# Kernel tuning notes

Measured on AMD Instinct MI355X. Metric: run time of the kernel, lower is better.

The kernel has to match this reference:

```python
import jax, jax.numpy as jnp
import numpy as np
from jax import lax

D = 1024  # inputSize == hidden size
B = 128   # batch
T = 256   # step


def setup_inputs() -> dict:
    key = jax.random.key(0)
    ks = jax.random.split(key, 9)
    s = 1.0 / np.sqrt(D)  # torch LSTMCell/Linear default init scale
    return {
        "inp": jax.random.normal(ks[0], (B, T, D), dtype=jnp.float32),
        "h0": jnp.zeros((B, D), dtype=jnp.float32),
        "c0": jnp.zeros((B, D), dtype=jnp.float32),
        "W_ih": jax.random.uniform(ks[1], (4 * D, D), jnp.float32, -s, s),
        "W_hh": jax.random.uniform(ks[2], (4 * D, D), jnp.float32, -s, s),
        "b_ih": jax.random.uniform(ks[3], (4 * D,), jnp.float32, -s, s),
        "b_hh": jax.random.uniform(ks[4], (4 * D,), jnp.float32, -s, s),
        "fc_w": jax.random.uniform(ks[5], (1, D), jnp.float32, -s, s),
        "fc_b": jax.random.uniform(ks[6], (1,), jnp.float32, -s, s),
        "step": T,
    }


def reference(inp, h0, c0, W_ih, W_hh, b_ih, b_hh, fc_w, fc_b, step):
    # The original's double python loop just transposes [B, T, D] -> [T, B, D].
    xs = jnp.swapaxes(inp, 0, 1)  # [T, B, D]

    def cell(carry, x):
        h, c = carry
        # torch.nn.LSTMCell gate order: i, f, g, o
        gates = x @ W_ih.T + b_ih + h @ W_hh.T + b_hh  # [B, 4D]
        i, f, g, o = jnp.split(gates, 4, axis=-1)
        i = jax.nn.sigmoid(i)
        f = jax.nn.sigmoid(f)
        g = jnp.tanh(g)
        o = jax.nn.sigmoid(o)
        c2 = f * c + i * g
        h2 = o * jnp.tanh(c2)
        return (h2, c2), None

    (hx, cx), _ = lax.scan(cell, (h0, c0), xs)
    yhat = jax.nn.sigmoid(hx @ fc_w.T + fc_b)  # [B, 1]
    return (yhat, hx, cx)
```

## Files before the change

kernel.cpp:

```cpp
#include <hip/hip_runtime.h>
#include <hip/hip_cooperative_groups.h>

namespace cg = cooperative_groups;

#define Dd 1024
#define Bb 128
#define Tt 256
#define NWG 256
#define NTHR 256

typedef short bf16x8 __attribute__((ext_vector_type(8)));
typedef float f32x4 __attribute__((ext_vector_type(4)));
typedef unsigned int u32x4 __attribute__((ext_vector_type(4)));
typedef unsigned long long u64;

static __device__ __forceinline__ unsigned short f2bf(float x) {
  unsigned int u = __float_as_uint(x);
  u += 0x7fffu + ((u >> 16) & 1u);
  return (unsigned short)(u >> 16);
}
static __device__ __forceinline__ unsigned int pk2(float a, float b) {
  return (unsigned int)f2bf(a) | ((unsigned int)f2bf(b) << 16);
}
static __device__ __forceinline__ bf16x8 as_bf(uint4 u) {
  union { uint4 u; bf16x8 v; } x; x.u = u; return x.v;
}
static __device__ __forceinline__ f32x4 mfma_(bf16x8 a, bf16x8 b, f32x4 c) {
  return __builtin_amdgcn_mfma_f32_16x16x32_bf16(a, b, c, 0, 0, 0);
}
static __device__ __forceinline__ float sigm(float x) { return 1.f / (1.f + __expf(-x)); }
static __device__ __forceinline__ float tanh_s(float x) { return 1.f - 2.f / (__expf(2.f * x) + 1.f); }
static __device__ __forceinline__ u64 aload(const u64* p) {
  return __hip_atomic_load(p, __ATOMIC_RELAXED, __HIP_MEMORY_SCOPE_AGENT);
}

template<int RING>
__global__ void __launch_bounds__(NTHR, 1) lstm_kernel(
    const float* __restrict__ inp, const float* __restrict__ h0,
    const float* __restrict__ c0, const float* __restrict__ W_ih,
    const float* __restrict__ W_hh, const float* __restrict__ b_ih,
    const float* __restrict__ b_hh, const float* __restrict__ fc_w,
    const float* __restrict__ fc_b, float* __restrict__ out,
    int* __restrict__ flags, unsigned short* __restrict__ hbuf,
    unsigned short* __restrict__ xbf, int use_xbf)
{
  extern __shared__ uint4 ldsW[];
  __shared__ float red[4];
  __shared__ int sent;

  const int tid = threadIdx.x;
  const int wg  = blockIdx.x;
  const int gid = wg * NTHR + tid;
  cg::grid_group grid = cg::this_grid();

  const int gs = wg >> 1;
  const int bh = wg & 1;

  if (tid < 4)
    __hip_atomic_store(&flags[bh * 512 + gs * 4 + tid], 0,
                       __ATOMIC_RELAXED, __HIP_MEMORY_SCOPE_AGENT);
  if (tid == 0) sent = -1;

  if (use_xbf) {
    for (int i = gid; i < Tt * Bb * (Dd / 8); i += NWG * NTHR) {
      int d8 = i & 127, b = (i >> 7) & 127, t = i >> 14;
      const float* s = inp + ((size_t)b * Tt + t) * Dd + d8 * 8;
      uint4 p;
      p.x = pk2(s[0], s[1]); p.y = pk2(s[2], s[3]);
      p.z = pk2(s[4], s[5]); p.w = pk2(s[6], s[7]);
      *(uint4*)(xbf + (size_t)i * 8) = p;
    }
  }
  uint4* hb4w = (uint4*)hbuf;
  for (int i = gid; i < 128 * 128; i += NWG * NTHR) {
    int row = i & 127, gsl = i >> 7;
    const float* s = h0 + (size_t)row * Dd + gsl * 8;
    uint4 p;
    p.x = pk2(s[0], s[1]); p.y = pk2(s[2], s[3]);
    p.z = pk2(s[4], s[5]); p.w = pk2(s[6], s[7]);
    hb4w[gsl * 128 + row] = p;
  }

  for (int i = tid; i < 8192; i += NTHR) {
    int l2 = i & 63, mmct = (i >> 6) & 3, kc = i >> 8;
    int cc = l2 & 15, ct = mmct & 1;
    int row = (((ct << 1) | (cc >> 3)) << 10) | (gs << 3) | (cc & 7);
    int k = kc * 32 + ((l2 >> 4) << 3);
    const float* s = ((mmct & 2) ? W_hh : W_ih) + (size_t)row * Dd + k;
    uint4 p;
    p.x = pk2(s[0], s[1]); p.y = pk2(s[2], s[3]);
    p.z = pk2(s[4], s[5]); p.w = pk2(s[6], s[7]);
    ldsW[i] = p;
  }

  const int w = tid >> 6, l = tid & 63;
  const int c = l & 15;
  const int rowbase = bh * 64 + w * 16;
  const int arow = rowbase + c;
  const int koff8 = l >> 4;
  const int r0 = ((c >> 3) << 10) | (gs << 3) | (c & 7);
  const int r1 = ((2 + (c >> 3)) << 10) | (gs << 3) | (c & 7);
  const float bias0 = b_ih[r0] + b_hh[r0];
  const float bias1 = b_ih[r1] + b_hh[r1];
  const int dim = (gs << 3) | (c & 7);
  const int crow = rowbase + (koff8 << 2);
  float creg[4];
  #pragma unroll
  for (int j = 0; j < 4; ++j) creg[j] = c0[(size_t)(crow + j) * Dd + dim];

  float* out_y = out;
  float* out_h = out + Bb;
  float* out_c = out + Bb + (size_t)Bb * Dd;

  int* myflag = &flags[bh * 512 + gs * 4 + w];
  const u64* fq = (const u64*)(flags + bh * 512);
  const int shbase = ((l & 15) >> 2) * 16;

  grid.sync();

  f32x4 pa0, pa1, pb0, pb1;

  {
    pa0 = f32x4{bias0, bias0, bias0, bias0};
    pa1 = f32x4{bias1, bias1, bias1, bias1};
    pb0 = f32x4{0.f, 0.f, 0.f, 0.f};
    pb1 = f32x4{0.f, 0.f, 0.f, 0.f};
    if (use_xbf) {
      const uint4* xA = (const uint4*)(xbf + ((size_t)0 * Bb + arow) * Dd + koff8 * 8);
      #pragma unroll
      for (int kc = 0; kc < 32; kc += 2) {
        uint4 ax0 = xA[kc * 4];
        uint4 ax1 = xA[(kc + 1) * 4];
        const int lb0 = kc * 256 + l, lb1 = (kc + 1) * 256 + l;
        pa0 = mfma_(as_bf(ax0), as_bf(ldsW[lb0]),      pa0);
        pa1 = mfma_(as_bf(ax0), as_bf(ldsW[lb0 + 64]), pa1);
        pb0 = mfma_(as_bf(ax1), as_bf(ldsW[lb1]),      pb0);
        pb1 = mfma_(as_bf(ax1), as_bf(ldsW[lb1 + 64]), pb1);
      }
    } else {
      const float* xF = inp + ((size_t)arow * Tt + 0) * Dd + koff8 * 8;
      #pragma unroll 4
      for (int kc = 0; kc < 32; ++kc) {
        const float* xs = xF + kc * 32;
        uint4 axu;
        axu.x = pk2(xs[0], xs[1]); axu.y = pk2(xs[2], xs[3]);
        axu.z = pk2(xs[4], xs[5]); axu.w = pk2(xs[6], xs[7]);
        const int lb = kc * 256 + l;
        pa0 = mfma_(as_bf(axu), as_bf(ldsW[lb]),      pa0);
        pa1 = mfma_(as_bf(axu), as_bf(ldsW[lb + 64]), pa1);
      }
    }
  }

  for (int t = 0; t < Tt; ++t) {
    const int rslot = RING ? t : (t & 1);
    const int wslot = RING ? (t + 1) : ((t + 1) & 1);

    if (w == 0) {
      int ok;
      do {
        u64 a = aload(&fq[l]);
        u64 b = aload(&fq[l + 64]);
        u64 c2 = aload(&fq[l + 128]);
        u64 d2 = aload(&fq[l + 192]);
        ok = ((int)a >= t) && ((int)(a >> 32) >= t) &&
             ((int)b >= t) && ((int)(b >> 32) >= t) &&
             ((int)c2 >= t) && ((int)(c2 >> 32) >= t) &&
             ((int)d2 >= t) && ((int)(d2 >> 32) >= t);
      } while (!__all(ok));
      __hip_atomic_store(&sent, t, __ATOMIC_RELEASE, __HIP_MEMORY_SCOPE_WORKGROUP);
    } else {
      while (__hip_atomic_load(&sent, __ATOMIC_ACQUIRE, __HIP_MEMORY_SCOPE_WORKGROUP) < t) {}
    }
    asm volatile("" ::: "memory");

    if constexpr (RING) {
      const uint4* hA4 = (const uint4*)(hbuf + (size_t)rslot * 131072);
      uint4 hc[8], hn[8];
      #pragma unroll
      for (int i = 0; i < 8; ++i) hc[i] = hA4[(i * 4 + koff8) * 128 + arow];
      #pragma unroll
      for (int oct = 0; oct < 4; ++oct) {
        if (oct < 3) {
          #pragma unroll
          for (int i = 0; i < 8; ++i)
            hn[i] = hA4[(((oct + 1) * 8 + i) * 4 + koff8) * 128 + arow];
        }
        #pragma unroll
        for (int i = 0; i < 8; i += 2) {
          const int kc = oct * 8 + i;
          const int lb0 = kc * 256 + l, lb1 = (kc + 1) * 256 + l;
          pa0 = mfma_(as_bf(hc[i]),     as_bf(ldsW[lb0 + 128]), pa0);
          pa1 = mfma_(as_bf(hc[i]),     as_bf(ldsW[lb0 + 192]), pa1);
          pb0 = mfma_(as_bf(hc[i + 1]), as_bf(ldsW[lb1 + 128]), pb0);
          pb1 = mfma_(as_bf(hc[i + 1]), as_bf(ldsW[lb1 + 192]), pb1);
        }
        if (oct < 3) {
          #pragma unroll
          for (int i = 0; i < 8; ++i) hc[i] = hn[i];
        }
      }
    } else {
      const u64* hA = (const u64*)hbuf + (size_t)rslot * 32768;
      #pragma unroll
      for (int kc = 0; kc < 32; kc += 2) {
        const int hi0 = (kc * 4 + koff8) * 256 + arow * 2;
        const int hi1 = ((kc + 1) * 4 + koff8) * 256 + arow * 2;
        union { u64 q[2]; uint4 p4; } h0u, h1u;
        h0u.q[0] = aload(&hA[hi0]); h0u.q[1] = aload(&hA[hi0 + 1]);
        h1u.q[0] = aload(&hA[hi1]); h1u.q[1] = aload(&hA[hi1 + 1]);
        const int lb0 = kc * 256 + l, lb1 = (kc + 1) * 256 + l;
        pa0 = mfma_(as_bf(h0u.p4), as_bf(ldsW[lb0 + 128]), pa0);
        pa1 = mfma_(as_bf(h0u.p4), as_bf(ldsW[lb0 + 192]), pa1);
        pb0 = mfma_(as_bf(h1u.p4), as_bf(ldsW[lb1 + 128]), pb0);
        pb1 = mfma_(as_bf(h1u.p4), as_bf(ldsW[lb1 + 192]), pb1);
      }
    }
    f32x4 acc0 = pa0 + pb0;
    f32x4 acc1 = pa1 + pb1;

    float fo0[4], fo1[4];
    #pragma unroll
    for (int j = 0; j < 4; ++j) {
      fo0[j] = __shfl_xor(acc0[j], 8);
      fo1[j] = __shfl_xor(acc1[j], 8);
    }
    unsigned int bfu0 = 0, bfu1 = 0, bfu2 = 0, bfu3 = 0;
    if (c < 8) {
      float hnv[4];
      #pragma unroll
      for (int j = 0; j < 4; ++j) {
        float iv = sigm(acc0[j]);
        float fv = sigm(fo0[j]);
        float gv = tanh_s(acc1[j]);
        float ov = sigm(fo1[j]);
        float cn = fv * creg[j] + iv * gv;
        float hn2 = ov * tanh_s(cn);
        creg[j] = cn;
        hnv[j] = hn2;
        if (t == Tt - 1) {
          size_t off = (size_t)(crow + j) * Dd + dim;
          __hip_atomic_store(&out_h[off], hn2, __ATOMIC_RELAXED, __HIP_MEMORY_SCOPE_AGENT);
          __hip_atomic_store(&out_c[off], cn, __ATOMIC_RELAXED, __HIP_MEMORY_SCOPE_AGENT);
        }
      }
      bfu0 = f2bf(hnv[0]); bfu1 = f2bf(hnv[1]);
      bfu2 = f2bf(hnv[2]); bfu3 = f2bf(hnv[3]);
    }

    unsigned int w0 = 0, w1 = 0, w2 = 0, w3 = 0;
    #pragma unroll
    for (int j = 0; j < 4; ++j) {
      unsigned int src = (j == 0) ? bfu0 : (j == 1) ? bfu1 : (j == 2) ? bfu2 : bfu3;
      unsigned int lo0 = __shfl((int)src, shbase + 0);
      unsigned int hi0g = __shfl((int)src, shbase + 1);
      unsigned int lo1 = __shfl((int)src, shbase + 2);
      unsigned int hi1g = __shfl((int)src, shbase + 3);
      unsigned int lo2 = __shfl((int)src, shbase + 4);
      unsigned int hi2g = __shfl((int)src, shbase + 5);
      unsigned int lo3 = __shfl((int)src, shbase + 6);
      unsigned int hi3g = __shfl((int)src, shbase + 7);
      bool mine = ((l & 3) == j);
      if (mine) {
        w0 = lo0 | (hi0g << 16);
        w1 = lo1 | (hi1g << 16);
        w2 = lo2 | (hi2g << 16);
        w3 = lo3 | (hi3g << 16);
      }
    }
    if (l < 16) {
      u32x4 val = {w0, w1, w2, w3};
      unsigned short* hw = hbuf + (size_t)wslot * 131072
                           + (size_t)gs * 1024 + (size_t)(rowbase + l) * 8;
      asm volatile("global_store_dwordx4 %0, %1, off sc0 sc1"
                   :: "v"(hw), "v"(val) : "memory");
    }

    pa0 = f32x4{bias0, bias0, bias0, bias0};
    pa1 = f32x4{bias1, bias1, bias1, bias1};
    pb0 = f32x4{0.f, 0.f, 0.f, 0.f};
    pb1 = f32x4{0.f, 0.f, 0.f, 0.f};
    if (t < Tt - 1) {
      if (use_xbf) {
        const uint4* xA = (const uint4*)(xbf + ((size_t)(t + 1) * Bb + arow) * Dd + koff8 * 8);
        #pragma unroll
        for (int kc = 0; kc < 32; kc += 2) {
          uint4 ax0 = xA[kc * 4];
          uint4 ax1 = xA[(kc + 1) * 4];
          const int lb0 = kc * 256 + l, lb1 = (kc + 1) * 256 + l;
          pa0 = mfma_(as_bf(ax0), as_bf(ldsW[lb0]),      pa0);
          pa1 = mfma_(as_bf(ax0), as_bf(ldsW[lb0 + 64]), pa1);
          pb0 = mfma_(as_bf(ax1), as_bf(ldsW[lb1]),      pb0);
          pb1 = mfma_(as_bf(ax1), as_bf(ldsW[lb1 + 64]), pb1);
        }
      } else {
        const float* xF = inp + ((size_t)arow * Tt + (t + 1)) * Dd + koff8 * 8;
        #pragma unroll 4
        for (int kc = 0; kc < 32; ++kc) {
          const float* xs = xF + kc * 32;
          uint4 axu;
          axu.x = pk2(xs[0], xs[1]); axu.y = pk2(xs[2], xs[3]);
          axu.z = pk2(xs[4], xs[5]); axu.w = pk2(xs[6], xs[7]);
          const int lb = kc * 256 + l;
          pa0 = mfma_(as_bf(axu), as_bf(ldsW[lb]),      pa0);
          pa1 = mfma_(as_bf(axu), as_bf(ldsW[lb + 64]), pa1);
        }
      }
    }

    asm volatile("s_waitcnt vmcnt(0)" ::: "memory");
    if (l == 0)
      __hip_atomic_store(myflag, t + 1, __ATOMIC_RELAXED, __HIP_MEMORY_SCOPE_AGENT);
  }

  if (wg < Bb) {
    {
      const u64* fa = (const u64*)flags;
      int ok;
      do {
        ok = 1;
        #pragma unroll
        for (int r = 0; r < 8; ++r) {
          u64 v = aload(&fa[l + r * 64]);
          ok &= ((int)v >= Tt) && ((int)(v >> 32) >= Tt);
        }
      } while (!__all(ok));
    }
    const u64* hr = (const u64*)(out_h + (size_t)wg * Dd);
    float s = 0.f;
    for (int k = tid; k < Dd / 2; k += NTHR) {
      u64 v = aload(&hr[k]);
      union { u64 u; float f[2]; } q; q.u = v;
      s += q.f[0] * fc_w[2 * k] + q.f[1] * fc_w[2 * k + 1];
    }
    #pragma unroll
    for (int off = 32; off > 0; off >>= 1) s += __shfl_down(s, off);
    if (l == 0) red[w] = s;
    __syncthreads();
    if (tid == 0) {
      float tot = red[0] + red[1] + red[2] + red[3] + fc_b[0];
      out_y[wg] = sigm(tot);
    }
  }
}

extern "C" void kernel_launch(void* const* d_in, const int* in_sizes, int n_in,
                              void* d_out, int out_size, void* d_ws, size_t ws_size,
                              hipStream_t stream) {
  (void)in_sizes; (void)n_in; (void)out_size;
  const float* inp  = (const float*)d_in[0];
  const float* h0   = (const float*)d_in[1];
  const float* c0   = (const float*)d_in[2];
  const float* W_ih = (const float*)d_in[3];
  const float* W_hh = (const float*)d_in[4];
  const float* b_ih = (const float*)d_in[5];
  const float* b_hh = (const float*)d_in[6];
  const float* fc_w = (const float*)d_in[7];
  const float* fc_b = (const float*)d_in[8];
  float* out = (float*)d_out;

  const size_t fbytes = 16384;
  const size_t slot   = (size_t)Bb * Dd * 2;
  const size_t ring1  = (size_t)(Tt + 1) * slot;
  const size_t ring0  = 2 * slot;
  const size_t xbytes = (size_t)Tt * Bb * Dd * 2;

  int ring, use_xbf;
  size_t rbytes;
  if (ws_size >= fbytes + ring1 + xbytes)      { ring = 1; use_xbf = 1; rbytes = ring1; }
  else if (ws_size >= fbytes + ring1)          { ring = 1; use_xbf = 0; rbytes = ring1; }
  else if (ws_size >= fbytes + ring0 + xbytes) { ring = 0; use_xbf = 1; rbytes = ring0; }
  else                                         { ring = 0; use_xbf = 0; rbytes = ring0; }

  int* flags = (int*)d_ws;
  unsigned short* hbuf = (unsigned short*)((char*)d_ws + fbytes);
  unsigned short* xbf  = (unsigned short*)((char*)d_ws + fbytes + rbytes);

  void* kfn = ring ? (void*)lstm_kernel<1> : (void*)lstm_kernel<0>;
  (void)hipFuncSetAttribute((const void*)kfn,
                            hipFuncAttributeMaxDynamicSharedMemorySize, 131072);

  void* kargs[] = {(void*)&inp, (void*)&h0, (void*)&c0, (void*)&W_ih, (void*)&W_hh,
                   (void*)&b_ih, (void*)&b_hh, (void*)&fc_w, (void*)&fc_b,
                   (void*)&out, (void*)&flags, (void*)&hbuf, (void*)&xbf, (void*)&use_xbf};
  (void)hipLaunchCooperativeKernel(kfn, dim3(NWG), dim3(NTHR),
                                   kargs, 131072u, stream);
}
```

Measured before the change: 2.914 ms.

## Merge batch halves into one 512-thread workgroup per gate slice

Switches from 256 workgroups of 256 threads, where each pair split the batch in half, to 128 workgroups of 512 threads, where each covers the full batch for its gate slice. This halves the number of flags each step barrier polls and shares the LDS weight tile across all 128 batch rows, which should lower global sync cost per timestep. It also drops the register-prefetched double-buffered h loads in favour of simple per-iteration loads. In exchange only 128 CUs are used, so per-CU MFMA and LDS work doubles, and h load latency may be less hidden.

```diff
diff --git a/kernel.cpp b/kernel.cpp
--- a/kernel.cpp
+++ b/kernel.cpp
@@ -6,8 +6,8 @@
 #define Dd 1024
 #define Bb 128
 #define Tt 256
-#define NWG 256
-#define NTHR 256
+#define NWG 128
+#define NTHR 512
 
 typedef short bf16x8 __attribute__((ext_vector_type(8)));
 typedef float f32x4 __attribute__((ext_vector_type(4)));
@@ -45,7 +45,7 @@
     unsigned short* __restrict__ xbf, int use_xbf)
 {
   extern __shared__ uint4 ldsW[];
-  __shared__ float red[4];
+  __shared__ float red[8];
   __shared__ int sent;
 
   const int tid = threadIdx.x;
@@ -53,11 +53,10 @@
   const int gid = wg * NTHR + tid;
   cg::grid_group grid = cg::this_grid();
 
-  const int gs = wg >> 1;
-  const int bh = wg & 1;
-
-  if (tid < 4)
-    __hip_atomic_store(&flags[bh * 512 + gs * 4 + tid], 0,
+  const int gs = wg;
+
+  if (tid < 8)
+    __hip_atomic_store(&flags[gs * 8 + tid], 0,
                        __ATOMIC_RELAXED, __HIP_MEMORY_SCOPE_AGENT);
   if (tid == 0) sent = -1;
 
@@ -95,7 +94,7 @@
 
   const int w = tid >> 6, l = tid & 63;
   const int c = l & 15;
-  const int rowbase = bh * 64 + w * 16;
+  const int rowbase = w * 16;
   const int arow = rowbase + c;
   const int koff8 = l >> 4;
   const int r0 = ((c >> 3) << 10) | (gs << 3) | (c & 7);
@@ -112,8 +111,8 @@
   float* out_h = out + Bb;
   float* out_c = out + Bb + (size_t)Bb * Dd;
 
-  int* myflag = &flags[bh * 512 + gs * 4 + w];
-  const u64* fq = (const u64*)(flags + bh * 512);
+  int* myflag = &flags[gs * 8 + w];
+  const u64* fq = (const u64*)flags;
   const int shbase = ((l & 15) >> 2) * 16;
 
   grid.sync();
@@ -161,12 +160,8 @@
       do {
         u64 a = aload(&fq[l]);
         u64 b = aload(&fq[l + 64]);
-        u64 c2 = aload(&fq[l + 128]);
-        u64 d2 = aload(&fq[l + 192]);
         ok = ((int)a >= t) && ((int)(a >> 32) >= t) &&
-             ((int)b >= t) && ((int)(b >> 32) >= t) &&
-             ((int)c2 >= t) && ((int)(c2 >> 32) >= t) &&
-             ((int)d2 >= t) && ((int)(d2 >> 32) >= t);
+             ((int)b >= t) && ((int)(b >> 32) >= t);
       } while (!__all(ok));
       __hip_atomic_store(&sent, t, __ATOMIC_RELEASE, __HIP_MEMORY_SCOPE_WORKGROUP);
     } else {
@@ -176,29 +171,15 @@
 
     if constexpr (RING) {
       const uint4* hA4 = (const uint4*)(hbuf + (size_t)rslot * 131072);
-      uint4 hc[8], hn[8];
-      #pragma unroll
-      for (int i = 0; i < 8; ++i) hc[i] = hA4[(i * 4 + koff8) * 128 + arow];
-      #pragma unroll
-      for (int oct = 0; oct < 4; ++oct) {
-        if (oct < 3) {
-          #pragma unroll
-          for (int i = 0; i < 8; ++i)
-            hn[i] = hA4[(((oct + 1) * 8 + i) * 4 + koff8) * 128 + arow];
-        }
-        #pragma unroll
-        for (int i = 0; i < 8; i += 2) {
-          const int kc = oct * 8 + i;
-          const int lb0 = kc * 256 + l, lb1 = (kc + 1) * 256 + l;
-          pa0 = mfma_(as_bf(hc[i]),     as_bf(ldsW[lb0 + 128]), pa0);
-          pa1 = mfma_(as_bf(hc[i]),     as_bf(ldsW[lb0 + 192]), pa1);
-          pb0 = mfma_(as_bf(hc[i + 1]), as_bf(ldsW[lb1 + 128]), pb0);
-          pb1 = mfma_(as_bf(hc[i + 1]), as_bf(ldsW[lb1 + 192]), pb1);
-        }
-        if (oct < 3) {
-          #pragma unroll
-          for (int i = 0; i < 8; ++i) hc[i] = hn[i];
-        }
+      #pragma unroll
+      for (int kc = 0; kc < 32; kc += 2) {
+        uint4 h0u = hA4[(kc * 4 + koff8) * 128 + arow];
+        uint4 h1u = hA4[((kc + 1) * 4 + koff8) * 128 + arow];
+        const int lb0 = kc * 256 + l, lb1 = (kc + 1) * 256 + l;
+        pa0 = mfma_(as_bf(h0u), as_bf(ldsW[lb0 + 128]), pa0);
+        pa1 = mfma_(as_bf(h0u), as_bf(ldsW[lb0 + 192]), pa1);
+        pb0 = mfma_(as_bf(h1u), as_bf(ldsW[lb1 + 128]), pb0);
+        pb1 = mfma_(as_bf(h1u), as_bf(ldsW[lb1 + 192]), pb1);
       }
     } else {
       const u64* hA = (const u64*)hbuf + (size_t)rslot * 32768;
@@ -313,17 +294,14 @@
       __hip_atomic_store(myflag, t + 1, __ATOMIC_RELAXED, __HIP_MEMORY_SCOPE_AGENT);
   }
 
-  if (wg < Bb) {
+  {
     {
-      const u64* fa = (const u64*)flags;
       int ok;
       do {
-        ok = 1;
-        #pragma unroll
-        for (int r = 0; r < 8; ++r) {
-          u64 v = aload(&fa[l + r * 64]);
-          ok &= ((int)v >= Tt) && ((int)(v >> 32) >= Tt);
-        }
+        u64 a = aload(&fq[l]);
+        u64 b = aload(&fq[l + 64]);
+        ok = ((int)a >= Tt) && ((int)(a >> 32) >= Tt) &&
+             ((int)b >= Tt) && ((int)(b >> 32) >= Tt);
       } while (!__all(ok));
     }
     const u64* hr = (const u64*)(out_h + (size_t)wg * Dd);
@@ -338,7 +316,9 @@
     if (l == 0) red[w] = s;
     __syncthreads();
     if (tid == 0) {
-      float tot = red[0] + red[1] + red[2] + red[3] + fc_b[0];
+      float tot = fc_b[0];
+      #pragma unroll
+      for (int i = 0; i < 8; ++i) tot += red[i];
       out_y[wg] = sigm(tot);
     }
   }
```

Result: slower. 4.622 ms (+58.6%).

## Precompute input projection in separate kernel, leaving only recurrent GEMM in scan

Applied to the files above, without the earlier changes.

Splits the monolithic LSTM kernel into three launches: a fp32-to-bf16 conversion of the input, a kernel that computes x@W_ih^T + biases for all timesteps into a bf16 gate buffer, and a cooperative scan kernel that only does h@W_hh^T per step and adds the precomputed gates. This takes the input-projection GEMM off the sequential critical path and halves the LDS weight footprint in the scan. The cost is extra global traffic for a large gate buffer, added launches, and an extra bf16 rounding of the input gates. It only runs when the workspace is large enough, otherwise it falls back to the old kernel. The ring path in the fallback also loses its hand-written h prefetch.

```diff
diff --git a/kernel.cpp b/kernel.cpp
--- a/kernel.cpp
+++ b/kernel.cpp
@@ -22,6 +22,9 @@
 static __device__ __forceinline__ unsigned int pk2(float a, float b) {
   return (unsigned int)f2bf(a) | ((unsigned int)f2bf(b) << 16);
 }
+static __device__ __forceinline__ float bf2f(unsigned int ubits) {
+  return __uint_as_float(ubits << 16);
+}
 static __device__ __forceinline__ bf16x8 as_bf(uint4 u) {
   union { uint4 u; bf16x8 v; } x; x.u = u; return x.v;
 }
@@ -34,8 +37,294 @@
   return __hip_atomic_load(p, __ATOMIC_RELAXED, __HIP_MEMORY_SCOPE_AGENT);
 }
 
+__global__ void xcvt_kernel(const float* __restrict__ inp,
+                            unsigned short* __restrict__ xbf)
+{
+  for (int i = blockIdx.x * 256 + threadIdx.x; i < Tt * Bb * (Dd / 8);
+       i += gridDim.x * 256) {
+    int d8 = i & 127, b = (i >> 7) & 127, t = i >> 14;
+    const float* s = inp + ((size_t)b * Tt + t) * Dd + d8 * 8;
+    uint4 p;
+    p.x = pk2(s[0], s[1]); p.y = pk2(s[2], s[3]);
+    p.z = pk2(s[4], s[5]); p.w = pk2(s[6], s[7]);
+    *(uint4*)(xbf + (size_t)i * 8) = p;
+  }
+}
+
+__global__ void __launch_bounds__(256, 1) xg_kernel(
+    const unsigned short* __restrict__ xbf, const float* __restrict__ W_ih,
+    const float* __restrict__ b_ih, const float* __restrict__ b_hh,
+    unsigned short* __restrict__ xg)
+{
+  extern __shared__ uint4 ldsW[];
+  const int tid = threadIdx.x;
+  const int wg  = blockIdx.x;
+  const int gs = wg >> 1;
+  const int bh = wg & 1;
+
+  for (int i = tid; i < 4096; i += 256) {
+    int l2 = i & 63, ct = (i >> 6) & 1, kc = i >> 7;
+    int cc = l2 & 15;
+    int row = (((ct << 1) | (cc >> 3)) << 10) | (gs << 3) | (cc & 7);
+    int k = kc * 32 + ((l2 >> 4) << 3);
+    const float* s = W_ih + (size_t)row * Dd + k;
+    uint4 p;
+    p.x = pk2(s[0], s[1]); p.y = pk2(s[2], s[3]);
+    p.z = pk2(s[4], s[5]); p.w = pk2(s[6], s[7]);
+    ldsW[i] = p;
+  }
+  __syncthreads();
+
+  const int w = tid >> 6, l = tid & 63;
+  const int c = l & 15;
+  const int rowbase = bh * 64 + w * 16;
+  const int arow = rowbase + c;
+  const int koff8 = l >> 4;
+  const int r0 = ((c >> 3) << 10) | (gs << 3) | (c & 7);
+  const int r1 = ((2 + (c >> 3)) << 10) | (gs << 3) | (c & 7);
+  const float bias0 = b_ih[r0] + b_hh[r0];
+  const float bias1 = b_ih[r1] + b_hh[r1];
+  const int crow = rowbase + (koff8 << 2);
+
+  for (int t = 0; t < Tt; ++t) {
+    f32x4 a0 = {bias0, bias0, bias0, bias0};
+    f32x4 a1 = {bias1, bias1, bias1, bias1};
+    f32x4 e0 = {0.f, 0.f, 0.f, 0.f};
+    f32x4 e1 = {0.f, 0.f, 0.f, 0.f};
+    const uint4* xA = (const uint4*)(xbf + ((size_t)t * Bb + arow) * Dd + koff8 * 8);
+    #pragma unroll
+    for (int kc = 0; kc < 32; kc += 2) {
+      uint4 ax0 = xA[kc * 4];
+      uint4 ax1 = xA[(kc + 1) * 4];
+      const int lb0 = kc * 128 + l, lb1 = (kc + 1) * 128 + l;
+      a0 = mfma_(as_bf(ax0), as_bf(ldsW[lb0]),      a0);
+      a1 = mfma_(as_bf(ax0), as_bf(ldsW[lb0 + 64]), a1);
+      e0 = mfma_(as_bf(ax1), as_bf(ldsW[lb1]),      e0);
+      e1 = mfma_(as_bf(ax1), as_bf(ldsW[lb1 + 64]), e1);
+    }
+    f32x4 s0 = a0 + e0;
+    f32x4 s1 = a1 + e1;
+    u64 q0 = (u64)pk2(s0[0], s0[1]) | ((u64)pk2(s0[2], s0[3]) << 32);
+    u64 q1 = (u64)pk2(s1[0], s1[1]) | ((u64)pk2(s1[2], s1[3]) << 32);
+    *(u64*)(xg + (size_t)t * 524288 + (size_t)r0 * 128 + crow) = q0;
+    *(u64*)(xg + (size_t)t * 524288 + (size_t)r1 * 128 + crow) = q1;
+  }
+}
+
+__global__ void __launch_bounds__(256, 1) lstm_scan_kernel(
+    const float* __restrict__ h0, const float* __restrict__ c0,
+    const float* __restrict__ W_hh, const float* __restrict__ fc_w,
+    const float* __restrict__ fc_b, float* __restrict__ out,
+    int* __restrict__ flags, unsigned short* __restrict__ hbuf,
+    const unsigned short* __restrict__ xg)
+{
+  extern __shared__ uint4 ldsW[];
+  __shared__ float red[4];
+  __shared__ int sent;
+
+  const int tid = threadIdx.x;
+  const int wg  = blockIdx.x;
+  const int gid = wg * 256 + tid;
+  cg::grid_group grid = cg::this_grid();
+
+  const int gs = wg >> 1;
+  const int bh = wg & 1;
+
+  if (tid < 4)
+    __hip_atomic_store(&flags[bh * 512 + gs * 4 + tid], 0,
+                       __ATOMIC_RELAXED, __HIP_MEMORY_SCOPE_AGENT);
+  if (tid == 0) sent = -1;
+
+  uint4* hb4w = (uint4*)hbuf;
+  for (int i = gid; i < 128 * 128; i += NWG * 256) {
+    int row = i & 127, gsl = i >> 7;
+    const float* s = h0 + (size_t)row * Dd + gsl * 8;
+    uint4 p;
+    p.x = pk2(s[0], s[1]); p.y = pk2(s[2], s[3]);
+    p.z = pk2(s[4], s[5]); p.w = pk2(s[6], s[7]);
+    hb4w[gsl * 128 + row] = p;
+  }
+
+  for (int i = tid; i < 4096; i += 256) {
+    int l2 = i & 63, ct = (i >> 6) & 1, kc = i >> 7;
+    int cc = l2 & 15;
+    int row = (((ct << 1) | (cc >> 3)) << 10) | (gs << 3) | (cc & 7);
+    int k = kc * 32 + ((l2 >> 4) << 3);
+    const float* s = W_hh + (size_t)row * Dd + k;
+    uint4 p;
+    p.x = pk2(s[0], s[1]); p.y = pk2(s[2], s[3]);
+    p.z = pk2(s[4], s[5]); p.w = pk2(s[6], s[7]);
+    ldsW[i] = p;
+  }
+
+  const int w = tid >> 6, l = tid & 63;
+  const int c = l & 15;
+  const int rowbase = bh * 64 + w * 16;
+  const int arow = rowbase + c;
+  const int koff8 = l >> 4;
+  const int r0 = ((c >> 3) << 10) | (gs << 3) | (c & 7);
+  const int r1 = ((2 + (c >> 3)) << 10) | (gs << 3) | (c & 7);
+  const int dim = (gs << 3) | (c & 7);
+  const int crow = rowbase + (koff8 << 2);
+  float creg[4];
+  #pragma unroll
+  for (int j = 0; j < 4; ++j) creg[j] = c0[(size_t)(crow + j) * Dd + dim];
+
+  float* out_y = out;
+  float* out_h = out + Bb;
+  float* out_c = out + Bb + (size_t)Bb * Dd;
+
+  int* myflag = &flags[bh * 512 + gs * 4 + w];
+  const u64* fq = (const u64*)(flags + bh * 512);
+  const int shbase = ((l & 15) >> 2) * 16;
+
+  grid.sync();
+
+  u64 xq0 = *(const u64*)(xg + (size_t)r0 * 128 + crow);
+  u64 xq1 = *(const u64*)(xg + (size_t)r1 * 128 + crow);
+
+  for (int t = 0; t < Tt; ++t) {
+    if (w == 0) {
+      int ok;
+      do {
+        u64 a = aload(&fq[l]);
+        u64 b = aload(&fq[l + 64]);
+        u64 c2 = aload(&fq[l + 128]);
+        u64 d2 = aload(&fq[l + 192]);
+        ok = ((int)a >= t) && ((int)(a >> 32) >= t) &&
+             ((int)b >= t) && ((int)(b >> 32) >= t) &&
+             ((int)c2 >= t) && ((int)(c2 >> 32) >= t) &&
+             ((int)d2 >= t) && ((int)(d2 >> 32) >= t);
+      } while (!__all(ok));
+      __hip_atomic_store(&sent, t, __ATOMIC_RELEASE, __HIP_MEMORY_SCOPE_WORKGROUP);
+    } else {
+      while (__hip_atomic_load(&sent, __ATOMIC_ACQUIRE, __HIP_MEMORY_SCOPE_WORKGROUP) < t) {}
+    }
+    asm volatile("" ::: "memory");
+
+    f32x4 pa0 = {0.f, 0.f, 0.f, 0.f};
+    f32x4 pa1 = {0.f, 0.f, 0.f, 0.f};
+    f32x4 pb0 = {0.f, 0.f, 0.f, 0.f};
+    f32x4 pb1 = {0.f, 0.f, 0.f, 0.f};
+    {
+      const uint4* hA4 = (const uint4*)(hbuf + (size_t)t * 131072);
+      #pragma unroll
+      for (int kc = 0; kc < 32; kc += 2) {
+        uint4 h0u = hA4[(kc * 4 + koff8) * 128 + arow];
+        uint4 h1u = hA4[((kc + 1) * 4 + koff8) * 128 + arow];
+        const int lb0 = kc * 128 + l, lb1 = (kc + 1) * 128 + l;
+        pa0 = mfma_(as_bf(h0u), as_bf(ldsW[lb0]),      pa0);
+        pa1 = mfma_(as_bf(h0u), as_bf(ldsW[lb0 + 64]), pa1);
+        pb0 = mfma_(as_bf(h1u), as_bf(ldsW[lb1]),      pb0);
+        pb1 = mfma_(as_bf(h1u), as_bf(ldsW[lb1 + 64]), pb1);
+      }
+    }
+    f32x4 acc0 = pa0 + pb0;
+    f32x4 acc1 = pa1 + pb1;
+    #pragma unroll
+    for (int j = 0; j < 4; ++j) {
+      acc0[j] += bf2f((unsigned int)(xq0 >> (16 * j)) & 0xffffu);
+      acc1[j] += bf2f((unsigned int)(xq1 >> (16 * j)) & 0xffffu);
+    }
+
+    float fo0[4], fo1[4];
+    #pragma unroll
+    for (int j = 0; j < 4; ++j) {
+      fo0[j] = __shfl_xor(acc0[j], 8);
+      fo1[j] = __shfl_xor(acc1[j], 8);
+    }
+    unsigned int bfu0 = 0, bfu1 = 0, bfu2 = 0, bfu3 = 0;
+    if (c < 8) {
+      float hnv[4];
+      #pragma unroll
+      for (int j = 0; j < 4; ++j) {
+        float iv = sigm(acc0[j]);
+        float fv = sigm(fo0[j]);
+        float gv = tanh_s(acc1[j]);
+        float ov = sigm(fo1[j]);
+        float cn = fv * creg[j] + iv * gv;
+        float hn2 = ov * tanh_s(cn);
+        creg[j] = cn;
+        hnv[j] = hn2;
+        if (t == Tt - 1) {
+          size_t off = (size_t)(crow + j) * Dd + dim;
+          __hip_atomic_store(&out_h[off], hn2, __ATOMIC_RELAXED, __HIP_MEMORY_SCOPE_AGENT);
+          __hip_atomic_store(&out_c[off], cn, __ATOMIC_RELAXED, __HIP_MEMORY_SCOPE_AGENT);
+        }
+      }
+      bfu0 = f2bf(hnv[0]); bfu1 = f2bf(hnv[1]);
+      bfu2 = f2bf(hnv[2]); bfu3 = f2bf(hnv[3]);
+    }
+
+    unsigned int w0 = 0, w1 = 0, w2 = 0, w3 = 0;
+    #pragma unroll
+    for (int j = 0; j < 4; ++j) {
+      unsigned int src = (j == 0) ? bfu0 : (j == 1) ? bfu1 : (j == 2) ? bfu2 : bfu3;
+      unsigned int lo0 = __shfl((int)src, shbase + 0);
+      unsigned int hi0g = __shfl((int)src, shbase + 1);
+      unsigned int lo1 = __shfl((int)src, shbase + 2);
+      unsigned int hi1g = __shfl((int)src, shbase + 3);
+      unsigned int lo2 = __shfl((int)src, shbase + 4);
+      unsigned int hi2g = __shfl((int)src, shbase + 5);
+      unsigned int lo3 = __shfl((int)src, shbase + 6);
+      unsigned int hi3g = __shfl((int)src, shbase + 7);
+      bool mine = ((l & 3) == j);
+      if (mine) {
+        w0 = lo0 | (hi0g << 16);
+        w1 = lo1 | (hi1g << 16);
+        w2 = lo2 | (hi2g << 16);
+        w3 = lo3 | (hi3g << 16);
+      }
+    }
+    if (l < 16) {
+      u32x4 val = {w0, w1, w2, w3};
+      unsigned short* hw = hbuf + (size_t)(t + 1) * 131072
+                           + (size_t)gs * 1024 + (size_t)(rowbase + l) * 8;
+      asm volatile("global_store_dwordx4 %0, %1, off sc0 sc1"
+                   :: "v"(hw), "v"(val) : "memory");
+    }
+    if (t + 1 < Tt) {
+      xq0 = *(const u64*)(xg + (size_t)(t + 1) * 524288 + (size_t)r0 * 128 + crow);
+      xq1 = *(const u64*)(xg + (size_t)(t + 1) * 524288 + (size_t)r1 * 128 + crow);
+    }
+    asm volatile("s_waitcnt vmcnt(0)" ::: "memory");
+    if (l == 0)
+      __hip_atomic_store(myflag, t + 1, __ATOMIC_RELAXED, __HIP_MEMORY_SCOPE_AGENT);
+  }
+
+  if (wg < Bb) {
+    {
+      const u64* fa = (const u64*)flags;
+      int ok;
+      do {
+        ok = 1;
+        #pragma unroll
+        for (int r = 0; r < 8; ++r) {
+          u64 v = aload(&fa[l + r * 64]);
+          ok &= ((int)v >= Tt) && ((int)(v >> 32) >= Tt);
+        }
+      } while (!__all(ok));
+    }
+    const u64* hr = (const u64*)(out_h + (size_t)wg * Dd);
+    float s = 0.f;
+    for (int k = tid; k < Dd / 2; k += 256) {
+      u64 v = aload(&hr[k]);
+      union { u64 u; float f[2]; } q; q.u = v;
+      s += q.f[0] * fc_w[2 * k] + q.f[1] * fc_w[2 * k + 1];
+    }
+    #pragma unroll
+    for (int off = 32; off > 0; off >>= 1) s += __shfl_down(s, off);
+    if (l == 0) red[w] = s;
+    __syncthreads();
+    if (tid == 0) {
+      float tot = red[0] + red[1] + red[2] + red[3] + fc_b[0];
+      out_y[wg] = sigm(tot);
+    }
+  }
+}
+
 template<int RING>
-__global__ void __launch_bounds__(NTHR, 1) lstm_kernel(
+__global__ void __launch_bounds__(NTHR, 1) lstm_kernel_mono(
     const float* __restrict__ inp, const float* __restrict__ h0,
     const float* __restrict__ c0, const float* __restrict__ W_ih,
     const float* __restrict__ W_hh, const float* __restrict__ b_ih,
@@ -80,7 +369,6 @@
     p.z = pk2(s[4], s[5]); p.w = pk2(s[6], s[7]);
     hb4w[gsl * 128 + row] = p;
   }
-
   for (int i = tid; i < 8192; i += NTHR) {
     int l2 = i & 63, mmct = (i >> 6) & 3, kc = i >> 8;
     int cc = l2 & 15, ct = mmct & 1;
@@ -119,7 +407,6 @@
   grid.sync();
 
   f32x4 pa0, pa1, pb0, pb1;
-
   {
     pa0 = f32x4{bias0, bias0, bias0, bias0};
     pa1 = f32x4{bias1, bias1, bias1, bias1};
@@ -176,29 +463,15 @@
 
     if constexpr (RING) {
       const uint4* hA4 = (const uint4*)(hbuf + (size_t)rslot * 131072);
-      uint4 hc[8], hn[8];
       #pragma unroll
-      for (int i = 0; i < 8; ++i) hc[i] = hA4[(i * 4 + koff8) * 128 + arow];
-      #pragma unroll
-      for (int oct = 0; oct < 4; ++oct) {
-        if (oct < 3) {
-          #pragma unroll
-          for (int i = 0; i < 8; ++i)
-            hn[i] = hA4[(((oct + 1) * 8 + i) * 4 + koff8) * 128 + arow];
-        }
-        #pragma unroll
-        for (int i = 0; i < 8; i += 2) {
-          const int kc = oct * 8 + i;
-          const int lb0 = kc * 256 + l, lb1 = (kc + 1) * 256 + l;
-          pa0 = mfma_(as_bf(hc[i]),     as_bf(ldsW[lb0 + 128]), pa0);
-          pa1 = mfma_(as_bf(hc[i]),     as_bf(ldsW[lb0 + 192]), pa1);
-          pb0 = mfma_(as_bf(hc[i + 1]), as_bf(ldsW[lb1 + 128]), pb0);
-          pb1 = mfma_(as_bf(hc[i + 1]), as_bf(ldsW[lb1 + 192]), pb1);
-        }
-        if (oct < 3) {
-          #pragma unroll
-          for (int i = 0; i < 8; ++i) hc[i] = hn[i];
-        }
+      for (int kc = 0; kc < 32; kc += 2) {
+        uint4 h0u = hA4[(kc * 4 + koff8) * 128 + arow];
+        uint4 h1u = hA4[((kc + 1) * 4 + koff8) * 128 + arow];
+        const int lb0 = kc * 256 + l, lb1 = (kc + 1) * 256 + l;
+        pa0 = mfma_(as_bf(h0u), as_bf(ldsW[lb0 + 128]), pa0);
+        pa1 = mfma_(as_bf(h0u), as_bf(ldsW[lb0 + 192]), pa1);
+        pb0 = mfma_(as_bf(h1u), as_bf(ldsW[lb1 + 128]), pb0);
+        pb1 = mfma_(as_bf(h1u), as_bf(ldsW[lb1 + 192]), pb1);
       }
     } else {
       const u64* hA = (const u64*)hbuf + (size_t)rslot * 32768;
@@ -359,11 +632,37 @@
   const float* fc_b = (const float*)d_in[8];
   float* out = (float*)d_out;
 
-  const size_t fbytes = 16384;
-  const size_t slot   = (size_t)Bb * Dd * 2;
-  const size_t ring1  = (size_t)(Tt + 1) * slot;
-  const size_t ring0  = 2 * slot;
-  const size_t xbytes = (size_t)Tt * Bb * Dd * 2;
+  const size_t fbytes  = 16384;
+  const size_t slot    = (size_t)Bb * Dd * 2;
+  const size_t ring1   = (size_t)(Tt + 1) * slot;
+  const size_t ring0   = 2 * slot;
+  const size_t xbytes  = (size_t)Tt * Bb * Dd * 2;
+  const size_t xgbytes = (size_t)Tt * 4096 * Bb * 2;
+
+  int* flags = (int*)d_ws;
+  unsigned short* hbuf = (unsigned short*)((char*)d_ws + fbytes);
+
+  if (ws_size >= fbytes + ring1 + xgbytes + xbytes) {
+    unsigned short* xg  = (unsigned short*)((char*)d_ws + fbytes + ring1);
+    unsigned short* xbf = (unsigned short*)((char*)d_ws + fbytes + ring1 + xgbytes);
+
+    hipLaunchKernelGGL(xcvt_kernel, dim3(2048), dim3(256), 0, stream, inp, xbf);
+
+    (void)hipFuncSetAttribute((const void*)xg_kernel,
+                              hipFuncAttributeMaxDynamicSharedMemorySize, 65536);
+    hipLaunchKernelGGL(xg_kernel, dim3(256), dim3(256), 65536, stream,
+                       xbf, W_ih, b_ih, b_hh, xg);
+
+    (void)hipFuncSetAttribute((const void*)lstm_scan_kernel,
+                              hipFuncAttributeMaxDynamicSharedMemorySize, 65536);
+    const unsigned short* xg_c = xg;
+    void* kargs[] = {(void*)&h0, (void*)&c0, (void*)&W_hh, (void*)&fc_w,
+                     (void*)&fc_b, (void*)&out, (void*)&flags, (void*)&hbuf,
+                     (void*)&xg_c};
+    (void)hipLaunchCooperativeKernel((void*)lstm_scan_kernel, dim3(NWG), dim3(NTHR),
+                                     kargs, 65536u, stream);
+    return;
+  }
 
   int ring, use_xbf;
   size_t rbytes;
@@ -372,11 +671,9 @@
   else if (ws_size >= fbytes + ring0 + xbytes) { ring = 0; use_xbf = 1; rbytes = ring0; }
   else                                         { ring = 0; use_xbf = 0; rbytes = ring0; }
 
-  int* flags = (int*)d_ws;
-  unsigned short* hbuf = (unsigned short*)((char*)d_ws + fbytes);
-  unsigned short* xbf  = (unsigned short*)((char*)d_ws + fbytes + rbytes);
-
-  void* kfn = ring ? (void*)lstm_kernel<1> : (void*)lstm_kernel<0>;
+  unsigned short* xbf = (unsigned short*)((char*)d_ws + fbytes + rbytes);
+
+  void* kfn = ring ? (void*)lstm_kernel_mono<1> : (void*)lstm_kernel_mono<0>;
   (void)hipFuncSetAttribute((const void*)kfn,
                             hipFuncAttributeMaxDynamicSharedMemorySize, 131072);
 
```

After: 4.213 ms. 44.5% more time.
